# Kernel tuning notes

Measured on AMD Instinct MI355X. Metric: run time of the kernel, lower is better.

Reference implementation:

```python
import jax, jax.numpy as jnp
import numpy as np

B, CIN, COUT, H, W = 2, 64, 64, 64, 2048
EPS = 1e-5


def unfold3(x):
    # x: [B, C, H, W] -> [B, H*W, 9, C], torch.nn.Unfold(k=3, pad=1) layout
    b, c, h, w = x.shape
    xp = jnp.pad(x, ((0, 0), (0, 0), (1, 1), (1, 1)))
    # kernel positions in row-major (ki, kj) order; index 4 is the center
    patches = jnp.stack([xp[:, :, i:i + h, j:j + w]
                         for i in range(3) for j in range(3)], axis=2)  # [B,C,9,H,W]
    return patches.reshape(b, c, 9, h * w).transpose(0, 3, 2, 1)  # [B,HW,9,C]


def setup_inputs() -> dict:
    key = jax.random.key(0)
    ks = jax.random.split(key, 8)
    x = jax.random.normal(ks[0], (B, 3 + CIN, H, W), dtype=jnp.float32)
    mask = jax.random.randint(ks[1], (B, 1, H, W), 0, 2, dtype=jnp.int32)
    w_spatial = jax.random.normal(ks[2], (CIN, 4), dtype=jnp.float32) * 0.5
    b_spatial = jax.random.normal(ks[3], (CIN,), dtype=jnp.float32) * 0.1
    w_channel = jax.random.normal(ks[4], (CIN, 4), dtype=jnp.float32) * 0.5
    b_channel = jax.random.normal(ks[5], (CIN,), dtype=jnp.float32) * 0.1
    w_agg = jax.random.normal(ks[6], (COUT, 9 * CIN), dtype=jnp.float32) * (1.0 / np.sqrt(9 * CIN))
    gamma = jnp.ones((COUT,), dtype=jnp.float32)
    beta = jnp.zeros((COUT,), dtype=jnp.float32)
    return {"x": x, "mask": mask, "w_spatial": w_spatial, "b_spatial": b_spatial,
            "w_channel": w_channel, "b_channel": b_channel, "w_agg": w_agg,
            "gamma": gamma, "beta": beta}


def reference(x, mask, w_spatial, b_spatial, w_channel, b_channel, w_agg, gamma, beta):
    b, _, h, w = x.shape
    x_un = unfold3(x)                              # [B,HW,9,3+C]
    feat = x_un[..., 3:]                           # [B,HW,9,C]
    x_pn = x_un[..., :3]                           # [B,HW,9,3]
    m_un = unfold3(mask.astype(jnp.float32))       # [B,HW,9,1]

    rng = jnp.linalg.norm(x_pn, axis=-1, keepdims=True)
    x_pn4 = jnp.concatenate([x_pn, rng], axis=-1)  # [B,HW,9,4]
    pn_p0 = x_pn4 - x_pn4[:, :, 4:5, :]            # relative to 3x3 center

    ws = jnp.einsum('bnkm,cm->bnkc', pn_p0, w_spatial) + b_spatial
    wc = jnp.einsum('bnkm,cm->bnkc', pn_p0, w_channel) + b_channel
    ws = jnp.max(ws, axis=3, keepdims=True)        # [B,HW,9,1]
    wc = jnp.max(wc, axis=2, keepdims=True)        # [B,HW,1,C]
    ws = jax.nn.softmax(ws, axis=2)
    wc = jax.nn.softmax(wc, axis=3)
    weights = (ws + wc) * m_un                     # [B,HW,9,C]

    feat = (weights * feat).reshape(b, h * w, 9 * CIN)
    out = jnp.einsum('bnf,of->bno', feat, w_agg)   # [B,HW,COUT]
    out = out.transpose(0, 2, 1)                   # [B,COUT,HW]

    # BatchNorm1d in training mode: stats over (batch, spatial) per channel
    mu = jnp.mean(out, axis=(0, 2), keepdims=True)
    var = jnp.mean((out - mu) ** 2, axis=(0, 2), keepdims=True)
    out = (out - mu) * jax.lax.rsqrt(var + EPS)
    out = out * gamma[None, :, None] + beta[None, :, None]
    out = jax.nn.relu(out)
    return out.reshape(b, COUT, h, w)              # Fold(k=1) == reshape
```

## Files before the change

### kernel.cpp

```cpp
#include <hip/hip_runtime.h>
#include <hip/hip_bf16.h>
#include <math.h>
#include <cstddef>

#define HDIM 64
#define WDIM 2048
#define HW   (HDIM*WDIM)
#define BATCH 2
#define CIN  64
#define COUT 64
#define XC   (3+CIN)
#define NPIX (BATCH*HW)
#define NBLK (NPIX/64)
#define NB2  (NBLK*2)
#define EPS  1e-5f

typedef short  short8  __attribute__((ext_vector_type(8)));
typedef float  f32x16  __attribute__((ext_vector_type(16)));

__device__ __forceinline__ unsigned short f2bf(float f) {
    unsigned int u = __float_as_uint(f);
    u += 0x7fff + ((u >> 16) & 1);
    return (unsigned short)(u >> 16);
}

struct __align__(16) SmemA {
    float wsm[9][64];
    float wcpart[4][64];
    float wcsum[4][64];
    unsigned int wcp[32][64];
    union {
        unsigned short V[64][72];
        float wspart[9][4][64];
    } u;
};

__global__ __launch_bounds__(256)
void kernelW(const float* __restrict__ w_agg, unsigned short* __restrict__ wbf)
{
    int t = blockIdx.x*256 + threadIdx.x;
    int co  = t / 72;
    int rem = t % 72;
    int kk  = rem >> 3;
    int ks  = (rem >> 1) & 3;
    int half= rem & 1;
    const float* src = w_agg + (size_t)co*576 + kk*64 + ks*16 + half*8;
    unsigned long long pk0 = 0, pk1 = 0;
    #pragma unroll
    for (int j=0;j<4;++j) pk0 |= (unsigned long long)f2bf(src[j])   << (16*j);
    #pragma unroll
    for (int j=0;j<4;++j) pk1 |= (unsigned long long)f2bf(src[4+j]) << (16*j);
    unsigned long long* dst =
        (unsigned long long*)(wbf + ((size_t)(((kk*4+ks)*2+half)*64 + co))*8);
    dst[0] = pk0; dst[1] = pk1;
}

__global__ __launch_bounds__(256, 4)
void kernelA(const float* __restrict__ x, const int* __restrict__ mask,
             const float* __restrict__ w_sp, const float* __restrict__ b_sp,
             const float* __restrict__ w_ch, const float* __restrict__ b_ch,
             const unsigned short* __restrict__ wbf,
             float* __restrict__ out, float* __restrict__ psum, float* __restrict__ psq)
{
    __shared__ SmemA s;
    const int tid = threadIdx.x;
    const int bid = blockIdx.x;
    const int b  = bid >> 11;
    const int r  = bid & 2047;
    const int h  = r >> 5;
    const int w0 = (r & 31) << 6;

    const int px = tid & 63;
    const int q  = tid >> 6;

    float p[9][4];
    float mkr[9];
    {
        const int wpix = w0 + px;
        #pragma unroll
        for (int k = 0; k < 9; ++k) {
            int hh = h + k/3 - 1;
            int ww = wpix + k%3 - 1;
            bool in = (hh >= 0) && (hh < HDIM) && (ww >= 0) && (ww < WDIM);
            float p0=0.f, p1=0.f, p2=0.f, mv=0.f;
            if (in) {
                size_t base = ((size_t)(b*XC)*HDIM + hh)*(size_t)WDIM + ww;
                p0 = x[base];
                p1 = x[base + (size_t)HW];
                p2 = x[base + 2*(size_t)HW];
                mv = (float)mask[((size_t)b*HDIM + hh)*(size_t)WDIM + ww];
            }
            p[k][0]=p0; p[k][1]=p1; p[k][2]=p2;
            p[k][3]=sqrtf(p0*p0 + p1*p1 + p2*p2);
            mkr[k]=mv;
        }
        float c0=p[4][0], c1=p[4][1], c2=p[4][2], c3=p[4][3];
        #pragma unroll
        for (int k = 0; k < 9; ++k) {
            p[k][0]-=c0; p[k][1]-=c1; p[k][2]-=c2; p[k][3]-=c3;
        }
    }

    float wsp[9];
    #pragma unroll
    for (int k=0;k<9;++k) wsp[k] = -1e30f;
    float wclog[16];
    float cqm = -1e30f;
    for (int cc = 0; cc < 16; ++cc) {
        int c = q*16 + cc;
        float a0=w_sp[c*4+0], a1=w_sp[c*4+1], a2=w_sp[c*4+2], a3=w_sp[c*4+3], bs=b_sp[c];
        float d0=w_ch[c*4+0], d1=w_ch[c*4+1], d2=w_ch[c*4+2], d3=w_ch[c*4+3], bc=b_ch[c];
        float tmax = bc;
        wsp[4] = fmaxf(wsp[4], bs);
        #pragma unroll
        for (int k=0;k<9;++k) {
            if (k == 4) continue;
            float sv = fmaf(p[k][0],a0, fmaf(p[k][1],a1, fmaf(p[k][2],a2, fmaf(p[k][3],a3, bs))));
            wsp[k] = fmaxf(wsp[k], sv);
            float tv = fmaf(p[k][0],d0, fmaf(p[k][1],d1, fmaf(p[k][2],d2, fmaf(p[k][3],d3, bc))));
            tmax = fmaxf(tmax, tv);
        }
        wclog[cc] = tmax;
        cqm = fmaxf(cqm, tmax);
    }
    #pragma unroll
    for (int k=0;k<9;++k) s.u.wspart[k][q][px] = wsp[k];
    s.wcpart[q][px] = cqm;
    __syncthreads();

    {
        float M = fmaxf(fmaxf(s.wcpart[0][px], s.wcpart[1][px]),
                        fmaxf(s.wcpart[2][px], s.wcpart[3][px]));
        float sum = 0.f;
        #pragma unroll
        for (int j=0; j<8; ++j) {
            float e0 = __expf(wclog[2*j]   - M);
            float e1 = __expf(wclog[2*j+1] - M);
            sum += e0 + e1;
            unsigned int u = (unsigned int)f2bf(e0) | ((unsigned int)f2bf(e1) << 16);
            s.wcp[q*8+j][px] = u;
        }
        s.wcsum[q][px] = sum;
    }
    if (q == 0) {
        float v[9]; float mx = -1e30f;
        #pragma unroll
        for (int k=0;k<9;++k) {
            float a = s.u.wspart[k][0][px];
            a = fmaxf(a, s.u.wspart[k][1][px]);
            a = fmaxf(a, s.u.wspart[k][2][px]);
            a = fmaxf(a, s.u.wspart[k][3][px]);
            v[k]=a; mx=fmaxf(mx,a);
        }
        float sum=0.f;
        #pragma unroll
        for (int k=0;k<9;++k) { v[k]=__expf(v[k]-mx); sum+=v[k]; }
        float inv = 1.0f/sum;
        #pragma unroll
        for (int k=0;k<9;++k) s.wsm[k][px] = v[k]*inv*mkr[k];
    }
    __syncthreads();

    const float winv = 1.0f / (s.wcsum[0][px] + s.wcsum[1][px] +
                               s.wcsum[2][px] + s.wcsum[3][px]);

    const int lane = tid & 63;
    const int wv   = tid >> 6;
    const int mrow = lane & 31;
    const int half = lane >> 5;
    const int co0  = (wv & 1) * 32;
    const int px0  = (wv >> 1) * 32;

    const short8* aswz = (const short8*)wbf;

    f32x16 acc;
    #pragma unroll
    for (int i=0;i<16;++i) acc[i]=0.f;

    for (int kk = 0; kk < 9; ++kk) {
        short8 af[4];
        #pragma unroll
        for (int ks=0; ks<4; ++ks)
            af[ks] = aswz[(size_t)(((kk*4+ks)*2+half)*64) + co0 + mrow];

        {
            int di = kk/3 - 1, dj = (kk%3) - 1;
            int hh = h + di;
            int ww = w0 + px + dj;
            bool inb = (hh>=0) && (hh<HDIM) && (ww>=0) && (ww<WDIM);
            int hhc = hh<0?0:(hh>HDIM-1?HDIM-1:hh);
            int wwc = ww<0?0:(ww>WDIM-1?WDIM-1:ww);
            const float* xb = x + ((size_t)(b*XC + 3)*HDIM + hhc)*(size_t)WDIM + wwc;
            float a_k = s.wsm[kk][px];
            float m2  = mkr[kk] * winv;
            unsigned int packed[8];
            #pragma unroll
            for (int j=0;j<8;++j) {
                unsigned c0 = 16u*q + 2u*j;
                unsigned int ew = s.wcp[q*8+j][px];
                float e0 = __uint_as_float(ew << 16);
                float e1 = __uint_as_float(ew & 0xffff0000u);
                float f0 = inb ? xb[(size_t)c0*HW]       : 0.f;
                float f1 = inb ? xb[(size_t)(c0+1)*HW]   : 0.f;
                float w0f = fmaf(m2, e0, a_k) * f0;
                float w1f = fmaf(m2, e1, a_k) * f1;
                __hip_bfloat162 h2 = __float22bfloat162_rn(float2{w0f, w1f});
                unsigned int u; __builtin_memcpy(&u, &h2, 4);
                packed[j] = u;
            }
            uint4* vp = (uint4*)&s.u.V[px][16*q];
            vp[0] = uint4{packed[0],packed[1],packed[2],packed[3]};
            vp[1] = uint4{packed[4],packed[5],packed[6],packed[7]};
        }
        __syncthreads();
        #pragma unroll
        for (int ks=0; ks<4; ++ks) {
            short8 bf = *(const short8*)&s.u.V[px0+mrow][ks*16 + half*8];
            acc = __builtin_amdgcn_mfma_f32_32x32x16_bf16(af[ks], bf, acc, 0, 0, 0);
        }
        __syncthreads();
    }

    const int pxg = w0 + px0 + mrow;
    #pragma unroll
    for (int reg=0; reg<16; ++reg) {
        int row = (reg&3) + 8*(reg>>2) + 4*half;
        int co  = co0 + row;
        float v = acc[reg];
        out[((size_t)(b*COUT+co))*HW + (size_t)h*WDIM + pxg] = v;
        float s1 = v, s2 = v*v;
        #pragma unroll
        for (int m=1; m<32; m<<=1) {
            s1 += __shfl_xor(s1, m, 64);
            s2 += __shfl_xor(s2, m, 64);
        }
        if (mrow == 0) {
            psum[(size_t)co*NB2 + bid*2 + (wv>>1)] = s1;
            psq [(size_t)co*NB2 + bid*2 + (wv>>1)] = s2;
        }
    }
}

__global__ __launch_bounds__(256)
void kernelB(const float* __restrict__ psum, const float* __restrict__ psq,
             float* __restrict__ stats)
{
    int co = blockIdx.x;
    int tid = threadIdx.x;
    float s=0.f, sq=0.f;
    for (int j = tid; j < NB2; j += 256) {
        s  += psum[(size_t)co*NB2 + j];
        sq += psq [(size_t)co*NB2 + j];
    }
    #pragma unroll
    for (int m=1; m<64; m<<=1) { s += __shfl_xor(s,m,64); sq += __shfl_xor(sq,m,64); }
    __shared__ float rs[4], rq[4];
    int wv = tid>>6;
    if ((tid&63)==0){ rs[wv]=s; rq[wv]=sq; }
    __syncthreads();
    if (tid==0) {
        float S = rs[0]+rs[1]+rs[2]+rs[3];
        float Q = rq[0]+rq[1]+rq[2]+rq[3];
        float mu = S / (float)NPIX;
        float var = Q/(float)NPIX - mu*mu;
        stats[co]      = mu;
        stats[64+co]   = rsqrtf(var + EPS);
    }
}

__global__ __launch_bounds__(256)
void kernelC(float* __restrict__ out, const float* __restrict__ stats,
             const float* __restrict__ gamma, const float* __restrict__ beta)
{
    size_t idx8 = (size_t)blockIdx.x*256 + threadIdx.x;
    size_t flat = idx8*8;
    int co = (int)((flat >> 17) & 63);
    float mu = stats[co], rstd = stats[64+co];
    float g  = gamma[co]*rstd;
    float bb = fmaf(-mu, g, beta[co]);
    #pragma unroll
    for (int t=0;t<2;++t) {
        float4 v = *(float4*)(out + flat + t*4);
        v.x = fmaxf(fmaf(v.x, g, bb), 0.f);
        v.y = fmaxf(fmaf(v.y, g, bb), 0.f);
        v.z = fmaxf(fmaf(v.z, g, bb), 0.f);
        v.w = fmaxf(fmaf(v.w, g, bb), 0.f);
        *(float4*)(out + flat + t*4) = v;
    }
}

extern "C" void kernel_launch(void* const* d_in, const int* in_sizes, int n_in,
                              void* d_out, int out_size, void* d_ws, size_t ws_size,
                              hipStream_t stream)
{
    const float* x     = (const float*)d_in[0];
    const int*   mask  = (const int*)  d_in[1];
    const float* w_sp  = (const float*)d_in[2];
    const float* b_sp  = (const float*)d_in[3];
    const float* w_ch  = (const float*)d_in[4];
    const float* b_ch  = (const float*)d_in[5];
    const float* w_agg = (const float*)d_in[6];
    const float* gamma = (const float*)d_in[7];
    const float* beta  = (const float*)d_in[8];
    float* out  = (float*)d_out;
    float* psum = (float*)d_ws;
    float* psq  = psum + (size_t)COUT*NB2;
    float* stats= psq  + (size_t)COUT*NB2;
    unsigned short* wbf = (unsigned short*)(stats + 128);

    kernelW<<<18, 256, 0, stream>>>(w_agg, wbf);
    kernelA<<<NBLK, 256, 0, stream>>>(x, mask, w_sp, b_sp, w_ch, b_ch, wbf, out, psum, psq);
    kernelB<<<COUT, 256, 0, stream>>>(psum, psq, stats);
    int grid_c = (NPIX*COUT/8)/256;
    kernelC<<<grid_c, 256, 0, stream>>>(out, stats, gamma, beta);
}
```

Before: 266.5 us.

## Stage 3-row feature halo tile in LDS as bf16 instead of 9 global gathers

Measured after the change: 317.0 us. 1.19x slower.

```diff
diff --git a/kernel.cpp b/kernel.cpp
--- a/kernel.cpp
+++ b/kernel.cpp
@@ -28,11 +28,11 @@
     float wsm[9][64];
     float wcpart[4][64];
     float wcsum[4][64];
-    unsigned int wcp[32][64];
     union {
-        unsigned short V[64][72];
+        unsigned short feat[12672];
         float wspart[9][4][64];
     } u;
+    unsigned short V[64][72];
 };
 
 __global__ __launch_bounds__(256)
@@ -128,17 +128,16 @@
     s.wcpart[q][px] = cqm;
     __syncthreads();
 
+    float ev[16];
     {
         float M = fmaxf(fmaxf(s.wcpart[0][px], s.wcpart[1][px]),
                         fmaxf(s.wcpart[2][px], s.wcpart[3][px]));
         float sum = 0.f;
         #pragma unroll
-        for (int j=0; j<8; ++j) {
-            float e0 = __expf(wclog[2*j]   - M);
-            float e1 = __expf(wclog[2*j+1] - M);
-            sum += e0 + e1;
-            unsigned int u = (unsigned int)f2bf(e0) | ((unsigned int)f2bf(e1) << 16);
-            s.wcp[q*8+j][px] = u;
+        for (int cc=0; cc<16; ++cc) {
+            float e = __expf(wclog[cc] - M);
+            ev[cc] = e;
+            sum += e;
         }
         s.wcsum[q][px] = sum;
     }
@@ -164,6 +163,32 @@
     const float winv = 1.0f / (s.wcsum[0][px] + s.wcsum[1][px] +
                                s.wcsum[2][px] + s.wcsum[3][px]);
 
+    for (int i = 0; i < 24; ++i) {
+        int task = q*24 + i;
+        int row  = task >> 5;
+        int c0   = (task & 31) * 2;
+        int hh   = h + row - 1;
+        bool rowOK = (hh >= 0) && (hh < HDIM);
+        int hhc = rowOK ? hh : 0;
+        const float* xb = x + ((size_t)(b*XC + 3 + c0)*HDIM + hhc)*(size_t)WDIM;
+        float v0 = rowOK ? xb[w0 + px]             : 0.f;
+        float v1 = rowOK ? xb[(size_t)HW + w0 + px]: 0.f;
+        unsigned int u = (unsigned int)f2bf(v0) | ((unsigned int)f2bf(v1) << 16);
+        int idx = ((row*66 + px + 1)*64 + c0) ^ (((px+1)&7)<<3);
+        *(unsigned int*)&s.u.feat[idx] = u;
+        if (px < 2) {
+            int pxi = (px==0) ? 0 : 65;
+            int ww  = (px==0) ? (w0-1) : (w0+64);
+            bool ok = rowOK && (ww >= 0) && (ww < WDIM);
+            float e0 = ok ? xb[ww]             : 0.f;
+            float e1 = ok ? xb[(size_t)HW + ww]: 0.f;
+            unsigned int ue = (unsigned int)f2bf(e0) | ((unsigned int)f2bf(e1) << 16);
+            int idxe = ((row*66 + pxi)*64 + c0) ^ ((pxi&7)<<3);
+            *(unsigned int*)&s.u.feat[idxe] = ue;
+        }
+    }
+    __syncthreads();
+
     const int lane = tid & 63;
     const int wv   = tid >> 6;
     const int mrow = lane & 31;
@@ -184,38 +209,45 @@
             af[ks] = aswz[(size_t)(((kk*4+ks)*2+half)*64) + co0 + mrow];
 
         {
-            int di = kk/3 - 1, dj = (kk%3) - 1;
-            int hh = h + di;
-            int ww = w0 + px + dj;
-            bool inb = (hh>=0) && (hh<HDIM) && (ww>=0) && (ww<WDIM);
-            int hhc = hh<0?0:(hh>HDIM-1?HDIM-1:hh);
-            int wwc = ww<0?0:(ww>WDIM-1?WDIM-1:ww);
-            const float* xb = x + ((size_t)(b*XC + 3)*HDIM + hhc)*(size_t)WDIM + wwc;
+            const int row = kk/3;
+            const int dj  = kk%3 - 1;
+            const int pxi = px + dj + 1;
+            const int fb  = (row*66 + pxi)*64;
+            const int swz = (pxi & 7) << 3;
+            union { short8 v; unsigned int u[4]; } fd0, fd1;
+            fd0.v = *(const short8*)&s.u.feat[(fb + 16*q)     ^ swz];
+            fd1.v = *(const short8*)&s.u.feat[(fb + 16*q + 8) ^ swz];
             float a_k = s.wsm[kk][px];
             float m2  = mkr[kk] * winv;
             unsigned int packed[8];
             #pragma unroll
-            for (int j=0;j<8;++j) {
-                unsigned c0 = 16u*q + 2u*j;
-                unsigned int ew = s.wcp[q*8+j][px];
-                float e0 = __uint_as_float(ew << 16);
-                float e1 = __uint_as_float(ew & 0xffff0000u);
-                float f0 = inb ? xb[(size_t)c0*HW]       : 0.f;
-                float f1 = inb ? xb[(size_t)(c0+1)*HW]   : 0.f;
-                float w0f = fmaf(m2, e0, a_k) * f0;
-                float w1f = fmaf(m2, e1, a_k) * f1;
+            for (int j=0;j<4;++j) {
+                float f0 = __uint_as_float(fd0.u[j] << 16);
+                float f1 = __uint_as_float(fd0.u[j] & 0xffff0000u);
+                float w0f = fmaf(m2, ev[2*j],   a_k) * f0;
+                float w1f = fmaf(m2, ev[2*j+1], a_k) * f1;
                 __hip_bfloat162 h2 = __float22bfloat162_rn(float2{w0f, w1f});
                 unsigned int u; __builtin_memcpy(&u, &h2, 4);
                 packed[j] = u;
             }
-            uint4* vp = (uint4*)&s.u.V[px][16*q];
+            #pragma unroll
+            for (int j=0;j<4;++j) {
+                float f0 = __uint_as_float(fd1.u[j] << 16);
+                float f1 = __uint_as_float(fd1.u[j] & 0xffff0000u);
+                float w0f = fmaf(m2, ev[8+2*j],   a_k) * f0;
+                float w1f = fmaf(m2, ev[8+2*j+1], a_k) * f1;
+                __hip_bfloat162 h2 = __float22bfloat162_rn(float2{w0f, w1f});
+                unsigned int u; __builtin_memcpy(&u, &h2, 4);
+                packed[4+j] = u;
+            }
+            uint4* vp = (uint4*)&s.V[px][16*q];
             vp[0] = uint4{packed[0],packed[1],packed[2],packed[3]};
             vp[1] = uint4{packed[4],packed[5],packed[6],packed[7]};
         }
         __syncthreads();
         #pragma unroll
         for (int ks=0; ks<4; ++ks) {
-            short8 bf = *(const short8*)&s.u.V[px0+mrow][ks*16 + half*8];
+            short8 bf = *(const short8*)&s.V[px0+mrow][ks*16 + half*8];
             acc = __builtin_amdgcn_mfma_f32_32x32x16_bf16(af[ks], bf, acc, 0, 0, 0);
         }
         __syncthreads();
```
